# Optimization experiments

Measured on AMD Instinct MI355X. Metric: run time of the kernel, lower is better.

The kernel has to match this reference:

```python
import jax, jax.numpy as jnp
import numpy as np
from jax import lax

LOOP = 100   # inferred: loop*16 == 16*100 reshape constraint
BN_EPS = 1e-5


def _swish(v):
    return v * jax.nn.sigmoid(v)


def setup_inputs() -> dict:
    key = jax.random.key(0)
    ks = jax.random.split(key, 9)
    f32 = jnp.float32
    return {
        "x": jax.random.normal(ks[0], (4, 4), f32),
        "conv_w": jax.random.normal(ks[1], (1, 1, 3, 3), f32) * 0.3,
        "conv_b": jax.random.normal(ks[2], (1,), f32) * 0.1,
        "bn_gamma": jnp.ones((1,), f32),
        "bn_beta": jnp.zeros((1,), f32),
        "bn_mean": jnp.zeros((1,), f32),
        "bn_var": jnp.ones((1,), f32),
        "w1": jax.random.normal(ks[3], (60, 100), f32) * 0.1,
        "b1": jax.random.normal(ks[4], (60,), f32) * 0.05,
        "w2": jax.random.normal(ks[5], (16, 60), f32) * 0.1,
        "b2": jax.random.normal(ks[6], (16,), f32) * 0.05,
        "w3": jax.random.normal(ks[7], (8, 16), f32) * 0.1,
        "b3": jax.random.normal(ks[8], (8,), f32) * 0.05,
    }


def reference(x, conv_w, conv_b, bn_gamma, bn_beta, bn_mean, bn_var,
              w1, b1, w2, b2, w3, b3):
    x0 = x.reshape(1, 1, 4, 4)
    inv_std = (bn_gamma / jnp.sqrt(bn_var + BN_EPS))[None, :, None, None]
    shift = (bn_beta)[None, :, None, None] - bn_mean[None, :, None, None] * inv_std
    cb = conv_b[None, :, None, None]

    def step(xc, _):
        # a = conv(x); b = BN(swish(conv(x)))  (same conv, same input -> same output)
        a = lax.conv_general_dilated(
            xc, conv_w, window_strides=(1, 1), padding='SAME',
            dimension_numbers=('NCHW', 'OIHW', 'NCHW')) + cb
        b = _swish(a) * inv_std + shift
        h = a * b
        xn = jnp.sign(h) * jnp.sqrt(jnp.abs(h))  # signed sqrt, vectorized
        return xn, xn

    _, kk = lax.scan(step, x0, None, length=LOOP)   # (LOOP, 1, 1, 4, 4)
    feats = kk.reshape(LOOP, 16).reshape(16, LOOP)  # flatten then reshape, as in torch

    h = feats @ w1.T + b1            # (16, 60)
    h = (_swish(h) - 0.5) / 0.5
    h = _swish(h @ w2.T + b2)        # (16, 16)
    y = h @ w3.T + b3                # (16, 8)
    return y
```

## Files before the change

kernel.cpp:

```cpp
#include <hip/hip_runtime.h>
#include <math.h>

#define LOOP 100
#define BN_EPS 1e-5f


__global__ __launch_bounds__(256) void model_kernel(
    const float* __restrict__ x,
    const float* __restrict__ conv_w,
    const float* __restrict__ conv_b,
    const float* __restrict__ bn_gamma,
    const float* __restrict__ bn_beta,
    const float* __restrict__ bn_mean,
    const float* __restrict__ bn_var,
    const float* __restrict__ w1,
    const float* __restrict__ b1,
    const float* __restrict__ w2,
    const float* __restrict__ b2,
    const float* __restrict__ w3,
    const float* __restrict__ b3,
    float* __restrict__ out)
{
    __shared__ float s_feats[1600];
    __shared__ float s_w1[6000];
    __shared__ float s_w2[960];
    __shared__ float s_w3[128];
    __shared__ float s_b1[64];
    __shared__ float s_b2[16];
    __shared__ float s_b3[8];
    __shared__ float s_a1[960];
    __shared__ float s_h2[256];

    const int tid = threadIdx.x;

    if (tid < 64) {
        const int p = tid;
        const int r = (p >> 2) & 3;
        const int c = p & 3;
        float xv = (p < 16) ? x[p] : 0.0f;

        float w[9];
        #pragma unroll
        for (int i = 0; i < 9; ++i) w[i] = conv_w[i];
        const float cb      = conv_b[0];
        const float inv_std = bn_gamma[0] / sqrtf(bn_var[0] + BN_EPS);
        const float shift   = bn_beta[0] - bn_mean[0] * inv_std;

        int   src[9];
        float msk[9];
        #pragma unroll
        for (int dr = -1; dr <= 1; ++dr) {
            #pragma unroll
            for (int dc = -1; dc <= 1; ++dc) {
                int i  = (dr + 1) * 3 + (dc + 1);
                int rr = r + dr, ccc = c + dc;
                bool ok = (p < 16) && rr >= 0 && rr < 4 && ccc >= 0 && ccc < 4;
                src[i] = ok ? (rr * 4 + ccc) : p;
                msk[i] = ok ? 1.0f : 0.0f;
            }
        }

        for (int k = 0; k < LOOP; ++k) {
            float v[9];
            #pragma unroll
            for (int i = 0; i < 9; ++i)
                v[i] = __shfl(xv, src[i], 64) * msk[i];
            float a = cb;
            #pragma unroll
            for (int i = 0; i < 9; ++i) a = fmaf(w[i], v[i], a);
            float t = expf(-a);
            float s = 1.0f / (1.0f + t);
            float b = fmaf(a * s, inv_std, shift);
            float h = a * b;
            float xn = copysignf(sqrtf(fabsf(h)), h);
            if (p < 16) s_feats[k * 16 + p] = xn;
            xv = xn;
        }
    } else {
        const int t = tid - 64;
        const float4* w1v = reinterpret_cast<const float4*>(w1);
        float4*       s1v = reinterpret_cast<float4*>(s_w1);
        for (int i = t; i < 1500; i += 192) s1v[i] = w1v[i];
        const float4* w2v = reinterpret_cast<const float4*>(w2);
        float4*       s2v = reinterpret_cast<float4*>(s_w2);
        for (int i = t; i < 240; i += 192) s2v[i] = w2v[i];
        if (t < 128) s_w3[t] = w3[t];
        if (t < 60)  s_b1[t] = b1[t];
        if (t < 16)  s_b2[t] = b2[t];
        if (t < 8)   s_b3[t] = b3[t];
    }
    __syncthreads();

    for (int q = tid; q < 960; q += 256) {
        int i = q / 60;
        int o = q - i * 60;
        const float4* fr = reinterpret_cast<const float4*>(&s_feats[i * 100]);
        const float4* wr = reinterpret_cast<const float4*>(&s_w1[o * 100]);
        float ax = 0.f, ay = 0.f, az = 0.f, aw = 0.f;
        #pragma unroll
        for (int j = 0; j < 25; ++j) {
            float4 f = fr[j], g = wr[j];
            ax = fmaf(f.x, g.x, ax);
            ay = fmaf(f.y, g.y, ay);
            az = fmaf(f.z, g.z, az);
            aw = fmaf(f.w, g.w, aw);
        }
        float acc = s_b1[o] + ((ax + ay) + (az + aw));
        float s = 1.0f / (1.0f + __expf(-acc));
        s_a1[q] = 2.0f * acc * s - 1.0f;
    }
    __syncthreads();

    {
        int i = tid >> 4;
        int o = tid & 15;
        const float4* ar = reinterpret_cast<const float4*>(&s_a1[i * 60]);
        const float4* wr = reinterpret_cast<const float4*>(&s_w2[o * 60]);
        float ax = 0.f, ay = 0.f, az = 0.f, aw = 0.f;
        #pragma unroll
        for (int j = 0; j < 15; ++j) {
            float4 f = ar[j], g = wr[j];
            ax = fmaf(f.x, g.x, ax);
            ay = fmaf(f.y, g.y, ay);
            az = fmaf(f.z, g.z, az);
            aw = fmaf(f.w, g.w, aw);
        }
        float acc = s_b2[o] + ((ax + ay) + (az + aw));
        float s = 1.0f / (1.0f + __expf(-acc));
        s_h2[tid] = acc * s;
    }
    __syncthreads();

    if (tid < 128) {
        int i = tid >> 3;
        int o = tid & 7;
        const float4* hr = reinterpret_cast<const float4*>(&s_h2[i * 16]);
        const float4* wr = reinterpret_cast<const float4*>(&s_w3[o * 16]);
        float ax = 0.f, ay = 0.f, az = 0.f, aw = 0.f;
        #pragma unroll
        for (int j = 0; j < 4; ++j) {
            float4 f = hr[j], g = wr[j];
            ax = fmaf(f.x, g.x, ax);
            ay = fmaf(f.y, g.y, ay);
            az = fmaf(f.z, g.z, az);
            aw = fmaf(f.w, g.w, aw);
        }
        out[i * 8 + o] = s_b3[o] + ((ax + ay) + (az + aw));
    }
}

extern "C" void kernel_launch(void* const* d_in, const int* in_sizes, int n_in,
                              void* d_out, int out_size, void* d_ws, size_t ws_size,
                              hipStream_t stream) {
    const float* x        = (const float*)d_in[0];
    const float* conv_w   = (const float*)d_in[1];
    const float* conv_b   = (const float*)d_in[2];
    const float* bn_gamma = (const float*)d_in[3];
    const float* bn_beta  = (const float*)d_in[4];
    const float* bn_mean  = (const float*)d_in[5];
    const float* bn_var   = (const float*)d_in[6];
    const float* w1       = (const float*)d_in[7];
    const float* b1       = (const float*)d_in[8];
    const float* w2       = (const float*)d_in[9];
    const float* b2       = (const float*)d_in[10];
    const float* w3       = (const float*)d_in[11];
    const float* b3       = (const float*)d_in[12];
    float* out = (float*)d_out;

    model_kernel<<<1, 256, 0, stream>>>(x, conv_w, conv_b, bn_gamma, bn_beta,
                                        bn_mean, bn_var, w1, b1, w2, b2, w3, b3, out);
}
```

Measured before the change: 99.21 us.

## Use DPP row shifts for stencil, fast intrinsics, and 4-output register blocking in layer1

Replaces the nine ds_bpermute-based shuffles in the serial 100-step conv recurrence with DPP row_shr/row_shl moves, which stay within 16-lane rows and have zero-fill for out-of-row lanes. Boundary masks are folded into the conv weights. The swish-BN product is algebraically rewritten, and it uses hardware rcp/sqrt and __expf instead of the precise library calls. Layer 1 is register-blocked so each thread computes four outputs sharing one feature row load, and the second and third sigmoids also switch to rcp. This shortens the latency-bound serial chain, at the cost of slightly reduced numerical precision.

```diff
diff --git a/kernel.cpp b/kernel.cpp
--- a/kernel.cpp
+++ b/kernel.cpp
@@ -3,6 +3,9 @@
 
 #define LOOP 100
 #define BN_EPS 1e-5f
+
+#define DPPF(v, ctrl) \
+    __int_as_float(__builtin_amdgcn_update_dpp(0, __float_as_int(v), (ctrl), 0xF, 0xF, true))
 
 
 __global__ __launch_bounds__(256) void model_kernel(
@@ -21,15 +24,15 @@
     const float* __restrict__ b3,
     float* __restrict__ out)
 {
-    __shared__ float s_feats[1600];
-    __shared__ float s_w1[6000];
-    __shared__ float s_w2[960];
-    __shared__ float s_w3[128];
-    __shared__ float s_b1[64];
-    __shared__ float s_b2[16];
-    __shared__ float s_b3[8];
-    __shared__ float s_a1[960];
-    __shared__ float s_h2[256];
+    __shared__ __align__(16) float s_feats[1664];
+    __shared__ __align__(16) float s_w1[6000];
+    __shared__ __align__(16) float s_w2[960];
+    __shared__ __align__(16) float s_w3[128];
+    __shared__ __align__(16) float s_b1[64];
+    __shared__ __align__(16) float s_b2[16];
+    __shared__ __align__(16) float s_b3[8];
+    __shared__ __align__(16) float s_a1[960];
+    __shared__ __align__(16) float s_h2[256];
 
     const int tid = threadIdx.x;
 
@@ -39,41 +42,51 @@
         const int c = p & 3;
         float xv = (p < 16) ? x[p] : 0.0f;
 
-        float w[9];
-        #pragma unroll
-        for (int i = 0; i < 9; ++i) w[i] = conv_w[i];
         const float cb      = conv_b[0];
         const float inv_std = bn_gamma[0] / sqrtf(bn_var[0] + BN_EPS);
         const float shift   = bn_beta[0] - bn_mean[0] * inv_std;
 
-        int   src[9];
-        float msk[9];
+        float wm[9];
         #pragma unroll
         for (int dr = -1; dr <= 1; ++dr) {
             #pragma unroll
             for (int dc = -1; dc <= 1; ++dc) {
                 int i  = (dr + 1) * 3 + (dc + 1);
-                int rr = r + dr, ccc = c + dc;
-                bool ok = (p < 16) && rr >= 0 && rr < 4 && ccc >= 0 && ccc < 4;
-                src[i] = ok ? (rr * 4 + ccc) : p;
-                msk[i] = ok ? 1.0f : 0.0f;
+                int rr = r + dr, cc2 = c + dc;
+                bool ok = (p < 16) && rr >= 0 && rr < 4 && cc2 >= 0 && cc2 < 4;
+                wm[i] = ok ? conv_w[i] : 0.0f;
             }
         }
 
         for (int k = 0; k < LOOP; ++k) {
-            float v[9];
-            #pragma unroll
-            for (int i = 0; i < 9; ++i)
-                v[i] = __shfl(xv, src[i], 64) * msk[i];
-            float a = cb;
-            #pragma unroll
-            for (int i = 0; i < 9; ++i) a = fmaf(w[i], v[i], a);
-            float t = expf(-a);
-            float s = 1.0f / (1.0f + t);
-            float b = fmaf(a * s, inv_std, shift);
-            float h = a * b;
-            float xn = copysignf(sqrtf(fabsf(h)), h);
-            if (p < 16) s_feats[k * 16 + p] = xn;
+            float vm5 = DPPF(xv, 0x115);
+            float vm4 = DPPF(xv, 0x114);
+            float vm3 = DPPF(xv, 0x113);
+            float vm1 = DPPF(xv, 0x111);
+            float vp1 = DPPF(xv, 0x101);
+            float vp3 = DPPF(xv, 0x103);
+            float vp4 = DPPF(xv, 0x104);
+            float vp5 = DPPF(xv, 0x105);
+
+            float a0 = fmaf(wm[0], vm5, cb);
+            a0 = fmaf(wm[3], vm1, a0);
+            a0 = fmaf(wm[6], vp3, a0);
+            float a1 = wm[1] * vm4;
+            a1 = fmaf(wm[4], xv, a1);
+            a1 = fmaf(wm[7], vp4, a1);
+            float a2 = wm[2] * vm3;
+            a2 = fmaf(wm[5], vp1, a2);
+            a2 = fmaf(wm[8], vp5, a2);
+            float a = (a0 + a1) + a2;
+
+            float e   = __expf(-a);
+            float s   = __builtin_amdgcn_rcpf(1.0f + e);
+            float t2  = a * a * inv_std;
+            float ash = a * shift;
+            float h   = fmaf(t2, s, ash);
+            float xn  = copysignf(__builtin_amdgcn_sqrtf(__builtin_fabsf(h)), h);
+
+            s_feats[k * 16 + p] = xn;
             xv = xn;
         }
     } else {
@@ -91,23 +104,35 @@
     }
     __syncthreads();
 
-    for (int q = tid; q < 960; q += 256) {
-        int i = q / 60;
-        int o = q - i * 60;
+    if (tid < 240) {
+        const int i  = tid / 15;
+        const int oq = tid - i * 15;
         const float4* fr = reinterpret_cast<const float4*>(&s_feats[i * 100]);
-        const float4* wr = reinterpret_cast<const float4*>(&s_w1[o * 100]);
-        float ax = 0.f, ay = 0.f, az = 0.f, aw = 0.f;
+        const float4* g[4] = {
+            reinterpret_cast<const float4*>(&s_w1[(oq     ) * 100]),
+            reinterpret_cast<const float4*>(&s_w1[(oq + 15) * 100]),
+            reinterpret_cast<const float4*>(&s_w1[(oq + 30) * 100]),
+            reinterpret_cast<const float4*>(&s_w1[(oq + 45) * 100]) };
+        float ax[4] = {0,0,0,0}, ay[4] = {0,0,0,0}, az[4] = {0,0,0,0}, aw[4] = {0,0,0,0};
         #pragma unroll
         for (int j = 0; j < 25; ++j) {
-            float4 f = fr[j], g = wr[j];
-            ax = fmaf(f.x, g.x, ax);
-            ay = fmaf(f.y, g.y, ay);
-            az = fmaf(f.z, g.z, az);
-            aw = fmaf(f.w, g.w, aw);
+            float4 f = fr[j];
+            #pragma unroll
+            for (int kk = 0; kk < 4; ++kk) {
+                float4 gg = g[kk][j];
+                ax[kk] = fmaf(f.x, gg.x, ax[kk]);
+                ay[kk] = fmaf(f.y, gg.y, ay[kk]);
+                az[kk] = fmaf(f.z, gg.z, az[kk]);
+                aw[kk] = fmaf(f.w, gg.w, aw[kk]);
+            }
         }
-        float acc = s_b1[o] + ((ax + ay) + (az + aw));
-        float s = 1.0f / (1.0f + __expf(-acc));
-        s_a1[q] = 2.0f * acc * s - 1.0f;
+        #pragma unroll
+        for (int kk = 0; kk < 4; ++kk) {
+            int o = oq + 15 * kk;
+            float acc = s_b1[o] + ((ax[kk] + ay[kk]) + (az[kk] + aw[kk]));
+            float s = __builtin_amdgcn_rcpf(1.0f + __expf(-acc));
+            s_a1[i * 60 + o] = 2.0f * acc * s - 1.0f;
+        }
     }
     __syncthreads();
 
@@ -119,14 +144,14 @@
         float ax = 0.f, ay = 0.f, az = 0.f, aw = 0.f;
         #pragma unroll
         for (int j = 0; j < 15; ++j) {
-            float4 f = ar[j], g = wr[j];
-            ax = fmaf(f.x, g.x, ax);
-            ay = fmaf(f.y, g.y, ay);
-            az = fmaf(f.z, g.z, az);
-            aw = fmaf(f.w, g.w, aw);
+            float4 f = ar[j], gg = wr[j];
+            ax = fmaf(f.x, gg.x, ax);
+            ay = fmaf(f.y, gg.y, ay);
+            az = fmaf(f.z, gg.z, az);
+            aw = fmaf(f.w, gg.w, aw);
         }
         float acc = s_b2[o] + ((ax + ay) + (az + aw));
-        float s = 1.0f / (1.0f + __expf(-acc));
+        float s = __builtin_amdgcn_rcpf(1.0f + __expf(-acc));
         s_h2[tid] = acc * s;
     }
     __syncthreads();
@@ -139,11 +164,11 @@
         float ax = 0.f, ay = 0.f, az = 0.f, aw = 0.f;
         #pragma unroll
         for (int j = 0; j < 4; ++j) {
-            float4 f = hr[j], g = wr[j];
-            ax = fmaf(f.x, g.x, ax);
-            ay = fmaf(f.y, g.y, ay);
-            az = fmaf(f.z, g.z, az);
-            aw = fmaf(f.w, g.w, aw);
+            float4 f = hr[j], gg = wr[j];
+            ax = fmaf(f.x, gg.x, ax);
+            ay = fmaf(f.y, gg.y, ay);
+            az = fmaf(f.z, gg.z, az);
+            aw = fmaf(f.w, gg.w, aw);
         }
         out[i * 8 + o] = s_b3[o] + ((ax + ay) + (az + aw));
     }
```

Result: faster. 85.61 us (-13.7%).
